# Performance work log

Hardware: AMD Instinct MI355X
Metric: run time of the kernel (lower is better)

The kernel has to match this reference:

```python
import jax, jax.numpy as jnp
import numpy as np

INPUT_DIM = 1024
HIDDEN_DIM = 1024


def setup_inputs() -> dict:
    key = jax.random.key(0)
    ks = jax.random.split(key, 7)
    s = 1.0 / np.sqrt(INPUT_DIM)
    x = jax.random.normal(ks[0], (4, 2048, INPUT_DIM), dtype=jnp.float32)
    Wq = jax.random.uniform(ks[1], (INPUT_DIM, HIDDEN_DIM), minval=-s, maxval=s, dtype=jnp.float32)
    bq = jax.random.uniform(ks[2], (HIDDEN_DIM,), minval=-s, maxval=s, dtype=jnp.float32)
    Wk = jax.random.uniform(ks[3], (INPUT_DIM, HIDDEN_DIM), minval=-s, maxval=s, dtype=jnp.float32)
    bk = jax.random.uniform(ks[4], (HIDDEN_DIM,), minval=-s, maxval=s, dtype=jnp.float32)
    Wv = jax.random.uniform(ks[5], (INPUT_DIM, HIDDEN_DIM), minval=-s, maxval=s, dtype=jnp.float32)
    bv = jax.random.uniform(ks[6], (HIDDEN_DIM,), minval=-s, maxval=s, dtype=jnp.float32)
    return {"x": x, "Wq": Wq, "bq": bq, "Wk": Wk, "bk": bk, "Wv": Wv, "bv": bv}


def reference(x, Wq, bq, Wk, bk, Wv, bv):
    # Q, K, V: [B, S, H]
    Q = jnp.einsum('bsd,dh->bsh', x, Wq) + bq
    K = jnp.einsum('bsd,dh->bsh', x, Wk) + bk
    V = jnp.einsum('bsd,dh->bsh', x, Wv) + bv
    scale = 1.0 / jnp.sqrt(jnp.array(Q.shape[-1], dtype=Q.dtype))
    scores = jnp.einsum('bqh,bkh->bqk', Q, K) * scale  # [B, S, S]
    attn = jax.nn.softmax(scores, axis=-1)
    return jnp.einsum('bqk,bkh->bqh', attn, V)
```

## Files before the change

kernel.cpp:

```cpp
#include <hip/hip_runtime.h>
#include <hip/hip_bf16.h>
#include <stdint.h>

typedef unsigned short u16;
typedef __attribute__((ext_vector_type(8))) short short8;
typedef __attribute__((ext_vector_type(4))) float floatx4;

#define BATCH 4
#define SEQ   2048
#define DIM   1024

__device__ inline u16 f2bf(float f) {
  union { float f; uint32_t u; } v; v.f = f;
  uint32_t r = v.u + 0x7fffu + ((v.u >> 16) & 1u);
  return (u16)(r >> 16);
}

__device__ inline uint32_t f2bf2(float lo, float hi) {
  __hip_bfloat162 h = __float22bfloat162_rn(float2{lo, hi});
  union { __hip_bfloat162 h; uint32_t u; } v; v.h = h;
  return v.u;
}

__device__ inline void gload_lds16(const u16* g, u16* l) {
  __builtin_amdgcn_global_load_lds((const __attribute__((address_space(1))) uint32_t*)g,
                                   (__attribute__((address_space(3))) uint32_t*)l,
                                   16, 0, 0);
}

__global__ __launch_bounds__(256) void prep(const float* __restrict__ x,
                                            const float* __restrict__ Wq,
                                            const float* __restrict__ Wk,
                                            const float* __restrict__ Wv,
                                            const float* __restrict__ bq,
                                            const float* __restrict__ bk,
                                            const float* __restrict__ bv,
                                            u16* __restrict__ Xb,
                                            u16* __restrict__ Wt,
                                            float* __restrict__ bias,
                                            float* __restrict__ lsum) {
  __shared__ u16 tile[32][33];
  const int bx = blockIdx.x;
  if (bx < 8192) {
    size_t i = ((size_t)bx * 256 + threadIdx.x) * 4;
    float4 v = *(const float4*)(x + i);
    uint2 o;
    o.x = f2bf2(v.x, v.y);
    o.y = f2bf2(v.z, v.w);
    *(uint2*)(Xb + i) = o;
    if (bx < 8) {
      float4 z = {0.f, 0.f, 0.f, 0.f};
      *(float4*)(lsum + (size_t)bx * 1024 + threadIdx.x * 4) = z;
    }
    return;
  }
  const int t = bx - 8192;
  const int tz = t >> 10;
  const int bxx = t & 31;
  const int byy = (t >> 5) & 31;
  const float* W = (tz == 0) ? Wq : (tz == 1) ? Wk : Wv;
  u16* o = Wt + (size_t)tz * (1u << 20);
  if (bxx == 0 && byy == 0) {
    const float* bsrc = (tz == 0) ? bq : (tz == 1) ? bk : bv;
    float4 b4 = *(const float4*)(bsrc + threadIdx.x * 4);
    *(float4*)(bias + tz * 1024 + threadIdx.x * 4) = b4;
  }
  int c0 = bxx * 32, r0 = byy * 32;
  int tx = threadIdx.x & 31, ty = threadIdx.x >> 5;
#pragma unroll
  for (int p = 0; p < 4; ++p)
    tile[p * 8 + ty][tx] = f2bf(W[(size_t)(r0 + p * 8 + ty) * DIM + c0 + tx]);
  __syncthreads();
#pragma unroll
  for (int p = 0; p < 4; ++p)
    o[(size_t)(c0 + p * 8 + ty) * DIM + r0 + tx] = tile[tx][p * 8 + ty];
}


__global__ __launch_bounds__(256, 4)
void qkv_fused(const u16* __restrict__ Xb, const u16* __restrict__ Wt,
               u16* __restrict__ Q, u16* __restrict__ Vt,
               const float* __restrict__ bias) {
  constexpr int K = 1024;
  __shared__ u16 ldsA[128 * 64];
  __shared__ u16 ldsB[128 * 64];
  const int lane = threadIdx.x & 63;
  const int wave = threadIdx.x >> 6;
  const int z = blockIdx.z;

  int mt, nt, N;
  const u16 *Ab, *Bb;
  if (z < 2) {
    mt = blockIdx.x; nt = blockIdx.y; N = 1024;
    Ab = Xb + (size_t)mt * 128 * K;
    Bb = Wt + (size_t)z * (1u << 20) + (size_t)nt * 128 * K;
  } else {
    nt = blockIdx.x; mt = blockIdx.y; N = 8192;
    Ab = Wt + (size_t)2 * (1u << 20) + (size_t)mt * 128 * K;
    Bb = Xb + (size_t)nt * 128 * K;
  }

  const int sr = lane >> 2;
  const int sc = ((lane & 3) ^ ((lane >> 3) & 3)) * 8;
  const u16* gA0 = Ab + (size_t)(wave * 32 + sr) * K + sc;
  const u16* gB0 = Bb + (size_t)(wave * 32 + sr) * K + sc;
  u16* lA0 = ldsA + wave * 1024;
  u16* lB0 = ldsB + wave * 1024;
  constexpr int SL = 4096;

  const int wm = (wave >> 1) * 64;
  const int wn = (wave & 1) * 64;
  const int fr = lane & 15;
  const int fk = ((lane >> 4) ^ ((fr >> 1) & 3)) * 8;
  const u16* la = ldsA + (wm + fr) * 32 + fk;
  const u16* lb = ldsB + (wn + fr) * 32 + fk;

  floatx4 acc[4][4] = {};

  for (int kt = 0; kt < K; kt += 64) {
    __syncthreads();
#pragma unroll
    for (int i = 0; i < 2; ++i) {
      gload_lds16(gA0 + kt + (size_t)(16 * i) * K, lA0 + i * 512);
      gload_lds16(gA0 + kt + 32 + (size_t)(16 * i) * K, lA0 + SL + i * 512);
      gload_lds16(gB0 + kt + (size_t)(16 * i) * K, lB0 + i * 512);
      gload_lds16(gB0 + kt + 32 + (size_t)(16 * i) * K, lB0 + SL + i * 512);
    }
    __syncthreads();
#pragma unroll
    for (int ks = 0; ks < 2; ++ks) {
      short8 a[4], b[4];
#pragma unroll
      for (int i = 0; i < 4; ++i) a[i] = *(const short8*)(la + ks * SL + i * 512);
#pragma unroll
      for (int i = 0; i < 4; ++i) b[i] = *(const short8*)(lb + ks * SL + i * 512);
#pragma unroll
      for (int mi = 0; mi < 4; ++mi)
#pragma unroll
        for (int ni = 0; ni < 4; ++ni)
          acc[mi][ni] = __builtin_amdgcn_mfma_f32_16x16x32_bf16(a[mi], b[ni], acc[mi][ni], 0, 0, 0);
    }
  }

  const int er = (lane >> 4) * 4;
  const int ec = lane & 15;
  const int r0 = mt * 128 + wm;
  const int c0 = nt * 128 + wn;

  if (z < 2) {
    u16* C = Q + (size_t)z * (8u << 20);
    const float* bz = bias + z * 1024;
    const float zs = (z == 0) ? 0.03125f : 1.0f;
#pragma unroll
    for (int mi = 0; mi < 4; ++mi)
#pragma unroll
      for (int ni = 0; ni < 4; ++ni) {
        const int col = c0 + ni * 16 + ec;
        const float bb = bz[col];
        const int row = r0 + mi * 16 + er;
        const uint32_t p0 = f2bf2((acc[mi][ni][0] + bb) * zs, (acc[mi][ni][1] + bb) * zs);
        const uint32_t p1 = f2bf2((acc[mi][ni][2] + bb) * zs, (acc[mi][ni][3] + bb) * zs);
        C[(size_t)(row + 0) * N + col] = (u16)p0;
        C[(size_t)(row + 1) * N + col] = (u16)(p0 >> 16);
        C[(size_t)(row + 2) * N + col] = (u16)p1;
        C[(size_t)(row + 3) * N + col] = (u16)(p1 >> 16);
      }
  } else {
    const float* bz = bias + 2 * 1024;
#pragma unroll
    for (int mi = 0; mi < 4; ++mi) {
      float bb[4];
#pragma unroll
      for (int r = 0; r < 4; ++r) bb[r] = bz[r0 + mi * 16 + er + r];
#pragma unroll
      for (int ni = 0; ni < 4; ++ni) {
        const int col = c0 + ni * 16 + ec;
        const size_t base = (size_t)(col >> 11) * (1u << 21) + (col & 2047);
        const int row = r0 + mi * 16 + er;
        const uint32_t p0 = f2bf2(acc[mi][ni][0] + bb[0], acc[mi][ni][1] + bb[1]);
        const uint32_t p1 = f2bf2(acc[mi][ni][2] + bb[2], acc[mi][ni][3] + bb[3]);
        Vt[base + (size_t)(row + 0) * 2048] = (u16)p0;
        Vt[base + (size_t)(row + 1) * 2048] = (u16)(p0 >> 16);
        Vt[base + (size_t)(row + 2) * 2048] = (u16)p1;
        Vt[base + (size_t)(row + 3) * 2048] = (u16)(p1 >> 16);
      }
    }
  }
}

template <int EPI, int SWIZ, int TM>
__global__ __launch_bounds__(256, (TM == 256) ? 2 : 4)
void gemm_bt(const u16* __restrict__ A, const u16* __restrict__ Bt,
             void* __restrict__ Cv, float* __restrict__ lsum,
             int M, int N, int K, size_t sA, size_t sB, size_t sC) {
  constexpr int MI = TM / 32;
  constexpr int AS = (TM >= 64) ? (TM / 64) : 1;
  __shared__ u16 ldsA[TM * 64];
  __shared__ u16 ldsB[128 * 64];
  const int lane = threadIdx.x & 63;
  const int wave = threadIdx.x >> 6;

  int mt, nt;
  {
    const int lin = blockIdx.x;
    const int c = lin & 7, j = lin >> 3;
    if (SWIZ == 5) {
      mt = 4 * (c >> 1) + (j & 3);
      nt = 8 * (c & 1) + (j >> 2);
    } else {
      mt = 8 * (c >> 1) + (j & 7);
      nt = 4 * (c & 1) + (j >> 3);
    }
  }

  const u16* Ab = A + sA * blockIdx.z + (size_t)mt * TM * K;
  const u16* Bb = Bt + sB * blockIdx.z + (size_t)nt * 128 * K;

  const int sr = lane >> 2;
  const int sc = ((lane & 3) ^ ((lane >> 3) & 3)) * 8;
  const u16* gA0 = Ab + (size_t)(wave * (TM / 4) + sr) * K + sc;
  const u16* gB0 = Bb + (size_t)(wave * 32 + sr) * K + sc;
  u16* lA0 = ldsA + wave * (TM / 4) * 32;
  u16* lB0 = ldsB + wave * 1024;
  constexpr int SLA = TM * 32;
  constexpr int SLB = 4096;

  const int wm = (wave >> 1) * (TM / 2);
  const int wn = (wave & 1) * 64;
  const int fr = lane & 15;
  const int fk = ((lane >> 4) ^ ((fr >> 1) & 3)) * 8;
  const u16* la = ldsA + (wm + fr) * 32 + fk;
  const u16* lb = ldsB + (wn + fr) * 32 + fk;

  floatx4 acc[MI][4] = {};

  for (int kt = 0; kt < K; kt += 64) {
    __syncthreads();
#pragma unroll
    for (int i = 0; i < AS; ++i) {
      gload_lds16(gA0 + kt + (size_t)(16 * i) * K, lA0 + i * 512);
      gload_lds16(gA0 + kt + 32 + (size_t)(16 * i) * K, lA0 + SLA + i * 512);
    }
#pragma unroll
    for (int i = 0; i < 2; ++i) {
      gload_lds16(gB0 + kt + (size_t)(16 * i) * K, lB0 + i * 512);
      gload_lds16(gB0 + kt + 32 + (size_t)(16 * i) * K, lB0 + SLB + i * 512);
    }
    __syncthreads();
#pragma unroll
    for (int ks = 0; ks < 2; ++ks) {
      short8 a[MI], b[4];
#pragma unroll
      for (int i = 0; i < MI; ++i)
        a[i] = *(const short8*)(la + ks * SLA + i * 512);
#pragma unroll
      for (int i = 0; i < 4; ++i)
        b[i] = *(const short8*)(lb + ks * SLB + i * 512);
#pragma unroll
      for (int mi = 0; mi < MI; ++mi)
#pragma unroll
        for (int ni = 0; ni < 4; ++ni)
          acc[mi][ni] = __builtin_amdgcn_mfma_f32_16x16x32_bf16(a[mi], b[ni], acc[mi][ni], 0, 0, 0);
    }
  }

  const int er = (lane >> 4) * 4;
  const int ec = lane & 15;
  const int r0 = mt * TM + wm;
  const int c0 = nt * 128 + wn;

  if (EPI == 1) {
    u16* C = (u16*)Cv + sC * blockIdx.z;
    float* lz = lsum + blockIdx.z * 2048;
#pragma unroll
    for (int mi = 0; mi < MI; ++mi) {
      float rs[4] = {0.f, 0.f, 0.f, 0.f};
#pragma unroll
      for (int ni = 0; ni < 4; ++ni) {
        const int col = c0 + ni * 16 + ec;
        const int row = r0 + mi * 16 + er;
        float e[4];
#pragma unroll
        for (int r = 0; r < 4; ++r) {
          e[r] = exp2f(acc[mi][ni][r] * 1.44269504088896340736f);
          rs[r] += e[r];
        }
        const uint32_t p0 = f2bf2(e[0], e[1]);
        const uint32_t p1 = f2bf2(e[2], e[3]);
        C[(size_t)(row + 0) * N + col] = (u16)p0;
        C[(size_t)(row + 1) * N + col] = (u16)(p0 >> 16);
        C[(size_t)(row + 2) * N + col] = (u16)p1;
        C[(size_t)(row + 3) * N + col] = (u16)(p1 >> 16);
      }
#pragma unroll
      for (int o = 1; o < 16; o <<= 1)
#pragma unroll
        for (int r = 0; r < 4; ++r) rs[r] += __shfl_xor(rs[r], o);
      if ((lane & 15) == 0) {
#pragma unroll
        for (int r = 0; r < 4; ++r)
          atomicAdd(&lz[r0 + mi * 16 + er + r], rs[r]);
      }
    }
  } else {
    float* C = (float*)Cv + sC * blockIdx.z;
    const float* lz = lsum + blockIdx.z * 2048;
#pragma unroll
    for (int mi = 0; mi < MI; ++mi) {
      float inv[4];
#pragma unroll
      for (int r = 0; r < 4; ++r) inv[r] = 1.0f / lz[r0 + mi * 16 + er + r];
#pragma unroll
      for (int ni = 0; ni < 4; ++ni) {
        const int col = c0 + ni * 16 + ec;
#pragma unroll
        for (int r = 0; r < 4; ++r) {
          const int row = r0 + mi * 16 + er + r;
          C[(size_t)row * N + col] = acc[mi][ni][r] * inv[r];
        }
      }
    }
  }
}

extern "C" void kernel_launch(void* const* d_in, const int* in_sizes, int n_in,
                              void* d_out, int out_size, void* d_ws, size_t ws_size,
                              hipStream_t stream) {
  const float* x  = (const float*)d_in[0];
  const float* Wq = (const float*)d_in[1];
  const float* bq = (const float*)d_in[2];
  const float* Wk = (const float*)d_in[3];
  const float* bk = (const float*)d_in[4];
  const float* Wv = (const float*)d_in[5];
  const float* bv = (const float*)d_in[6];
  float* out = (float*)d_out;

  char* ws = (char*)d_ws;
  const size_t MB = 1ull << 20;
  u16* Q    = (u16*)(ws + 0 * MB);
  u16* Kb   = (u16*)(ws + 16 * MB);
  u16* Vt   = (u16*)(ws + 48 * MB);
  u16* Xb   = (u16*)(ws + 64 * MB);
  u16* Wt   = (u16*)(ws + 80 * MB);
  float* bias = (float*)(ws + 86 * MB);
  float* lsum = (float*)(ws + 87 * MB);
  u16* P    = (u16*)(ws + 88 * MB);
  (void)Kb; (void)ws_size; (void)in_sizes; (void)n_in; (void)out_size;

  prep<<<11264, 256, 0, stream>>>(x, Wq, Wk, Wv, bq, bk, bv, Xb, Wt, bias, lsum);
  qkv_fused<<<dim3(64, 8, 3), 256, 0, stream>>>(Xb, Wt, Q, Vt, bias);
  gemm_bt<1, 5, 128><<<dim3(256, 1, 4), 256, 0, stream>>>(
      Q, Kb, P, lsum, 2048, 2048, 1024,
      (size_t)2097152, (size_t)2097152, (size_t)4194304);
  gemm_bt<2, 6, 64><<<dim3(256, 1, 4), 256, 0, stream>>>(
      P, Vt, out, lsum, 2048, 1024, 2048,
      (size_t)4194304, (size_t)2097152, (size_t)2097152);
}
```

Baseline: 236.1 us.

## Fuse score and PV GEMMs into one cooperative kernel with grid sync

```diff
diff --git a/kernel.cpp b/kernel.cpp
--- a/kernel.cpp
+++ b/kernel.cpp
@@ -1,6 +1,9 @@
 #include <hip/hip_runtime.h>
+#include <hip/hip_cooperative_groups.h>
 #include <hip/hip_bf16.h>
 #include <stdint.h>
+
+namespace cg = cooperative_groups;
 
 typedef unsigned short u16;
 typedef __attribute__((ext_vector_type(8))) short short8;
@@ -77,6 +80,59 @@
 }
 
 
+template <int TM, int K>
+__device__ __forceinline__ void kloop(const u16* __restrict__ Ab, const u16* __restrict__ Bb,
+                                      u16* __restrict__ ldsA, u16* __restrict__ ldsB,
+                                      int lane, int wave, floatx4 (&acc)[TM / 32][4]) {
+  constexpr int MI = TM / 32;
+  constexpr int AS = TM / 64;
+  const int sr = lane >> 2;
+  const int sc = ((lane & 3) ^ ((lane >> 3) & 3)) * 8;
+  const u16* gA0 = Ab + (size_t)(wave * (TM / 4) + sr) * K + sc;
+  const u16* gB0 = Bb + (size_t)(wave * 32 + sr) * K + sc;
+  u16* lA0 = ldsA + wave * (TM / 4) * 32;
+  u16* lB0 = ldsB + wave * 1024;
+  constexpr int SLA = TM * 32;
+  constexpr int SLB = 4096;
+
+  const int wm = (wave >> 1) * (TM / 2);
+  const int wn = (wave & 1) * 64;
+  const int fr = lane & 15;
+  const int fk = ((lane >> 4) ^ ((fr >> 1) & 3)) * 8;
+  const u16* la = ldsA + (wm + fr) * 32 + fk;
+  const u16* lb = ldsB + (wn + fr) * 32 + fk;
+
+  for (int kt = 0; kt < K; kt += 64) {
+    __syncthreads();
+#pragma unroll
+    for (int i = 0; i < AS; ++i) {
+      gload_lds16(gA0 + kt + (size_t)(16 * i) * K, lA0 + i * 512);
+      gload_lds16(gA0 + kt + 32 + (size_t)(16 * i) * K, lA0 + SLA + i * 512);
+    }
+#pragma unroll
+    for (int i = 0; i < 2; ++i) {
+      gload_lds16(gB0 + kt + (size_t)(16 * i) * K, lB0 + i * 512);
+      gload_lds16(gB0 + kt + 32 + (size_t)(16 * i) * K, lB0 + SLB + i * 512);
+    }
+    __syncthreads();
+#pragma unroll
+    for (int ks = 0; ks < 2; ++ks) {
+      short8 a[MI], b[4];
+#pragma unroll
+      for (int i = 0; i < MI; ++i)
+        a[i] = *(const short8*)(la + ks * SLA + i * 512);
+#pragma unroll
+      for (int i = 0; i < 4; ++i)
+        b[i] = *(const short8*)(lb + ks * SLB + i * 512);
+#pragma unroll
+      for (int mi = 0; mi < MI; ++mi)
+#pragma unroll
+        for (int ni = 0; ni < 4; ++ni)
+          acc[mi][ni] = __builtin_amdgcn_mfma_f32_16x16x32_bf16(a[mi], b[ni], acc[mi][ni], 0, 0, 0);
+    }
+  }
+}
+
 __global__ __launch_bounds__(256, 4)
 void qkv_fused(const u16* __restrict__ Xb, const u16* __restrict__ Wt,
                u16* __restrict__ Q, u16* __restrict__ Vt,
@@ -100,48 +156,11 @@
     Bb = Xb + (size_t)nt * 128 * K;
   }
 
-  const int sr = lane >> 2;
-  const int sc = ((lane & 3) ^ ((lane >> 3) & 3)) * 8;
-  const u16* gA0 = Ab + (size_t)(wave * 32 + sr) * K + sc;
-  const u16* gB0 = Bb + (size_t)(wave * 32 + sr) * K + sc;
-  u16* lA0 = ldsA + wave * 1024;
-  u16* lB0 = ldsB + wave * 1024;
-  constexpr int SL = 4096;
+  floatx4 acc[4][4] = {};
+  kloop<128, 1024>(Ab, Bb, ldsA, ldsB, lane, wave, acc);
 
   const int wm = (wave >> 1) * 64;
   const int wn = (wave & 1) * 64;
-  const int fr = lane & 15;
-  const int fk = ((lane >> 4) ^ ((fr >> 1) & 3)) * 8;
-  const u16* la = ldsA + (wm + fr) * 32 + fk;
-  const u16* lb = ldsB + (wn + fr) * 32 + fk;
-
-  floatx4 acc[4][4] = {};
-
-  for (int kt = 0; kt < K; kt += 64) {
-    __syncthreads();
-#pragma unroll
-    for (int i = 0; i < 2; ++i) {
-      gload_lds16(gA0 + kt + (size_t)(16 * i) * K, lA0 + i * 512);
-      gload_lds16(gA0 + kt + 32 + (size_t)(16 * i) * K, lA0 + SL + i * 512);
-      gload_lds16(gB0 + kt + (size_t)(16 * i) * K, lB0 + i * 512);
-      gload_lds16(gB0 + kt + 32 + (size_t)(16 * i) * K, lB0 + SL + i * 512);
-    }
-    __syncthreads();
-#pragma unroll
-    for (int ks = 0; ks < 2; ++ks) {
-      short8 a[4], b[4];
-#pragma unroll
-      for (int i = 0; i < 4; ++i) a[i] = *(const short8*)(la + ks * SL + i * 512);
-#pragma unroll
-      for (int i = 0; i < 4; ++i) b[i] = *(const short8*)(lb + ks * SL + i * 512);
-#pragma unroll
-      for (int mi = 0; mi < 4; ++mi)
-#pragma unroll
-        for (int ni = 0; ni < 4; ++ni)
-          acc[mi][ni] = __builtin_amdgcn_mfma_f32_16x16x32_bf16(a[mi], b[ni], acc[mi][ni], 0, 0, 0);
-    }
-  }
-
   const int er = (lane >> 4) * 4;
   const int ec = lane & 15;
   const int r0 = mt * 128 + wm;
@@ -188,13 +207,108 @@
   }
 }
 
+__global__ __launch_bounds__(256, 4)
+void score_pv(const u16* __restrict__ Q, u16* __restrict__ P,
+              const u16* __restrict__ Vt, float* __restrict__ out,
+              float* __restrict__ lsum) {
+  __shared__ u16 ldsA[128 * 64];
+  __shared__ u16 ldsB[128 * 64];
+  const int lane = threadIdx.x & 63;
+  const int wave = threadIdx.x >> 6;
+  const int bid = blockIdx.x;
+  const int z = bid >> 8;
+  const int q = bid & 255;
+  const int c = q & 7, j = q >> 3;
+  const int er = (lane >> 4) * 4;
+  const int ec = lane & 15;
+
+  {
+    const int mt = 4 * (c >> 1) + (j & 3);
+    const int nt = 8 * (c & 1) + (j >> 2);
+    const u16* Ab = Q + (size_t)z * 2097152 + (size_t)mt * 128 * 1024;
+    const u16* Bb = Q + 8388608 + (size_t)z * 2097152 + (size_t)nt * 128 * 1024;
+    floatx4 acc[4][4] = {};
+    kloop<128, 1024>(Ab, Bb, ldsA, ldsB, lane, wave, acc);
+
+    const int wm = (wave >> 1) * 64;
+    const int wn = (wave & 1) * 64;
+    const int r0 = mt * 128 + wm;
+    const int c0 = nt * 128 + wn;
+    u16* C = P + (size_t)z * 4194304;
+    float* lz = lsum + z * 2048;
+#pragma unroll
+    for (int mi = 0; mi < 4; ++mi) {
+      float rs[4] = {0.f, 0.f, 0.f, 0.f};
+#pragma unroll
+      for (int ni = 0; ni < 4; ++ni) {
+        const int col = c0 + ni * 16 + ec;
+        const int row = r0 + mi * 16 + er;
+        float e[4];
+#pragma unroll
+        for (int r = 0; r < 4; ++r) {
+          e[r] = exp2f(acc[mi][ni][r] * 1.44269504088896340736f);
+          rs[r] += e[r];
+        }
+        const uint32_t p0 = f2bf2(e[0], e[1]);
+        const uint32_t p1 = f2bf2(e[2], e[3]);
+        C[(size_t)(row + 0) * 2048 + col] = (u16)p0;
+        C[(size_t)(row + 1) * 2048 + col] = (u16)(p0 >> 16);
+        C[(size_t)(row + 2) * 2048 + col] = (u16)p1;
+        C[(size_t)(row + 3) * 2048 + col] = (u16)(p1 >> 16);
+      }
+#pragma unroll
+      for (int o = 1; o < 16; o <<= 1)
+#pragma unroll
+        for (int r = 0; r < 4; ++r) rs[r] += __shfl_xor(rs[r], o);
+      if ((lane & 15) == 0) {
+#pragma unroll
+        for (int r = 0; r < 4; ++r)
+          atomicAdd(&lz[r0 + mi * 16 + er + r], rs[r]);
+      }
+    }
+  }
+
+  __threadfence();
+  cg::this_grid().sync();
+
+  {
+    const int mt = 8 * (c >> 1) + (j & 7);
+    const int nt = 4 * (c & 1) + (j >> 3);
+    const u16* Ab = P + (size_t)z * 4194304 + (size_t)mt * 64 * 2048;
+    const u16* Bb = Vt + (size_t)z * 2097152 + (size_t)nt * 128 * 2048;
+    floatx4 acc[2][4] = {};
+    kloop<64, 2048>(Ab, Bb, ldsA, ldsB, lane, wave, acc);
+
+    const int wm = (wave >> 1) * 32;
+    const int wn = (wave & 1) * 64;
+    const int r0 = mt * 64 + wm;
+    const int c0 = nt * 128 + wn;
+    float* C = out + (size_t)z * 2097152;
+    const float* lz = lsum + z * 2048;
+#pragma unroll
+    for (int mi = 0; mi < 2; ++mi) {
+      float inv[4];
+#pragma unroll
+      for (int r = 0; r < 4; ++r) inv[r] = 1.0f / lz[r0 + mi * 16 + er + r];
+#pragma unroll
+      for (int ni = 0; ni < 4; ++ni) {
+        const int col = c0 + ni * 16 + ec;
+#pragma unroll
+        for (int r = 0; r < 4; ++r) {
+          const int row = r0 + mi * 16 + er + r;
+          C[(size_t)row * 1024 + col] = acc[mi][ni][r] * inv[r];
+        }
+      }
+    }
+  }
+}
+
 template <int EPI, int SWIZ, int TM>
-__global__ __launch_bounds__(256, (TM == 256) ? 2 : 4)
+__global__ __launch_bounds__(256, 4)
 void gemm_bt(const u16* __restrict__ A, const u16* __restrict__ Bt,
              void* __restrict__ Cv, float* __restrict__ lsum,
              int M, int N, int K, size_t sA, size_t sB, size_t sC) {
   constexpr int MI = TM / 32;
-  constexpr int AS = (TM >= 64) ? (TM / 64) : 1;
   __shared__ u16 ldsA[TM * 64];
   __shared__ u16 ldsB[128 * 64];
   const int lane = threadIdx.x & 63;
@@ -204,66 +318,19 @@
   {
     const int lin = blockIdx.x;
     const int c = lin & 7, j = lin >> 3;
-    if (SWIZ == 5) {
-      mt = 4 * (c >> 1) + (j & 3);
-      nt = 8 * (c & 1) + (j >> 2);
-    } else {
-      mt = 8 * (c >> 1) + (j & 7);
-      nt = 4 * (c & 1) + (j >> 3);
-    }
+    if (SWIZ == 5) { mt = 4 * (c >> 1) + (j & 3); nt = 8 * (c & 1) + (j >> 2); }
+    else           { mt = 8 * (c >> 1) + (j & 7); nt = 4 * (c & 1) + (j >> 3); }
   }
 
   const u16* Ab = A + sA * blockIdx.z + (size_t)mt * TM * K;
   const u16* Bb = Bt + sB * blockIdx.z + (size_t)nt * 128 * K;
 
-  const int sr = lane >> 2;
-  const int sc = ((lane & 3) ^ ((lane >> 3) & 3)) * 8;
-  const u16* gA0 = Ab + (size_t)(wave * (TM / 4) + sr) * K + sc;
-  const u16* gB0 = Bb + (size_t)(wave * 32 + sr) * K + sc;
-  u16* lA0 = ldsA + wave * (TM / 4) * 32;
-  u16* lB0 = ldsB + wave * 1024;
-  constexpr int SLA = TM * 32;
-  constexpr int SLB = 4096;
+  floatx4 acc[MI][4] = {};
+  if (K == 1024) kloop<TM, 1024>(Ab, Bb, ldsA, ldsB, lane, wave, acc);
+  else           kloop<TM, 2048>(Ab, Bb, ldsA, ldsB, lane, wave, acc);
 
   const int wm = (wave >> 1) * (TM / 2);
   const int wn = (wave & 1) * 64;
-  const int fr = lane & 15;
-  const int fk = ((lane >> 4) ^ ((fr >> 1) & 3)) * 8;
-  const u16* la = ldsA + (wm + fr) * 32 + fk;
-  const u16* lb = ldsB + (wn + fr) * 32 + fk;
-
-  floatx4 acc[MI][4] = {};
-
-  for (int kt = 0; kt < K; kt += 64) {
-    __syncthreads();
-#pragma unroll
-    for (int i = 0; i < AS; ++i) {
-      gload_lds16(gA0 + kt + (size_t)(16 * i) * K, lA0 + i * 512);
-      gload_lds16(gA0 + kt + 32 + (size_t)(16 * i) * K, lA0 + SLA + i * 512);
-    }
-#pragma unroll
-    for (int i = 0; i < 2; ++i) {
-      gload_lds16(gB0 + kt + (size_t)(16 * i) * K, lB0 + i * 512);
-      gload_lds16(gB0 + kt + 32 + (size_t)(16 * i) * K, lB0 + SLB + i * 512);
-    }
-    __syncthreads();
-#pragma unroll
-    for (int ks = 0; ks < 2; ++ks) {
-      short8 a[MI], b[4];
-#pragma unroll
-      for (int i = 0; i < MI; ++i)
-        a[i] = *(const short8*)(la + ks * SLA + i * 512);
-#pragma unroll
-      for (int i = 0; i < 4; ++i)
-        b[i] = *(const short8*)(lb + ks * SLB + i * 512);
-#pragma unroll
-      for (int mi = 0; mi < MI; ++mi)
-#pragma unroll
-        for (int ni = 0; ni < 4; ++ni)
-          acc[mi][ni] = __builtin_amdgcn_mfma_f32_16x16x32_bf16(a[mi], b[ni], acc[mi][ni], 0, 0, 0);
-    }
-  }
-
   const int er = (lane >> 4) * 4;
   const int ec = lane & 15;
   const int r0 = mt * TM + wm;
@@ -349,10 +416,18 @@
 
   prep<<<11264, 256, 0, stream>>>(x, Wq, Wk, Wv, bq, bk, bv, Xb, Wt, bias, lsum);
   qkv_fused<<<dim3(64, 8, 3), 256, 0, stream>>>(Xb, Wt, Q, Vt, bias);
-  gemm_bt<1, 5, 128><<<dim3(256, 1, 4), 256, 0, stream>>>(
-      Q, Kb, P, lsum, 2048, 2048, 1024,
-      (size_t)2097152, (size_t)2097152, (size_t)4194304);
-  gemm_bt<2, 6, 64><<<dim3(256, 1, 4), 256, 0, stream>>>(
-      P, Vt, out, lsum, 2048, 1024, 2048,
-      (size_t)4194304, (size_t)2097152, (size_t)2097152);
-}
+  {
+    const u16* Qa = Q; u16* Pa = P; const u16* Va = Vt; float* oa = out; float* la = lsum;
+    void* args[] = {(void*)&Qa, (void*)&Pa, (void*)&Va, (void*)&oa, (void*)&la};
+    hipError_t e = hipLaunchCooperativeKernel((const void*)score_pv, dim3(1024), dim3(256),
+                                              args, 0, stream);
+    if (e != hipSuccess) {
+      gemm_bt<1, 5, 128><<<dim3(256, 1, 4), 256, 0, stream>>>(
+          Q, Kb, P, lsum, 2048, 2048, 1024,
+          (size_t)2097152, (size_t)2097152, (size_t)4194304);
+      gemm_bt<2, 6, 64><<<dim3(256, 1, 4), 256, 0, stream>>>(
+          P, Vt, out, lsum, 2048, 1024, 2048,
+          (size_t)4194304, (size_t)2097152, (size_t)2097152);
+    }
+  }
+}
```

Measured after the change: 517.6 us. +119.2%, slower.
